# Kernel tuning notes

Measured on AMD Instinct MI355X. Metric: run time of the kernel, lower is better.

The kernel has to match this reference:

```python
import jax, jax.numpy as jnp
import numpy as np

B = 128
C_IN = 1
HID = 256
LAT = 256
NC = 4096
NA = 16
G = 4
DH = 256        # DynamicsModel default hidden_dim
CE = DH // 2    # code/action embed dim
IMG = 64
COMMIT = 0.25
DN = ('NCHW', 'OIHW', 'NCHW')


def conv_s2(x, w, b):
    y = jax.lax.conv_general_dilated(x, w, (2, 2), ((1, 1), (1, 1)), dimension_numbers=DN)
    return y + b[None, :, None, None]


def deconv_s2(x, w, b):
    # torch ConvTranspose2d(k=4, s=2, p=1): flip kernel, swap I/O channels,
    wt = jnp.flip(w, (2, 3)).transpose(1, 0, 2, 3)
    y = jax.lax.conv_general_dilated(x, wt, (1, 1), ((2, 2), (2, 2)),
                                     lhs_dilation=(2, 2), dimension_numbers=DN)
    return y + b[None, :, None, None]


def setup_inputs():
    key = jax.random.key(0)
    ks = iter(jax.random.split(key, 64))

    def W(shape, fan_in):
        return jax.random.normal(next(ks), shape, jnp.float32) * np.float32(1.0 / np.sqrt(fan_in))

    inp = {}
    inp['x'] = jax.random.uniform(next(ks), (B, C_IN, IMG, IMG), jnp.float32)
    inp['x_next'] = jax.random.uniform(next(ks), (B, C_IN, IMG, IMG), jnp.float32)
    inp['action'] = jax.random.randint(next(ks), (B,), 0, NA)
    # encoder Conv2d weights: [out, in, 4, 4]
    inp['enc_w1'] = W((HID, C_IN, 4, 4), C_IN * 16); inp['enc_b1'] = jnp.zeros((HID,), jnp.float32)
    inp['enc_w2'] = W((HID, HID, 4, 4), HID * 16);   inp['enc_b2'] = jnp.zeros((HID,), jnp.float32)
    inp['enc_w3'] = W((HID, HID, 4, 4), HID * 16);   inp['enc_b3'] = jnp.zeros((HID,), jnp.float32)
    inp['enc_w4'] = W((LAT, HID, 4, 4), HID * 16);   inp['enc_b4'] = jnp.zeros((LAT,), jnp.float32)
    # decoder ConvTranspose2d weights: [in, out, 4, 4]
    inp['dec_w1'] = W((LAT, HID, 4, 4), LAT * 4);    inp['dec_b1'] = jnp.zeros((HID,), jnp.float32)
    inp['dec_w2'] = W((HID, HID, 4, 4), HID * 4);    inp['dec_b2'] = jnp.zeros((HID,), jnp.float32)
    inp['dec_w3'] = W((HID, HID, 4, 4), HID * 4);    inp['dec_b3'] = jnp.zeros((HID,), jnp.float32)
    inp['dec_w4'] = W((HID, C_IN, 4, 4), HID * 4);   inp['dec_b4'] = jnp.zeros((C_IN,), jnp.float32)
    inp['codebook'] = jax.random.normal(next(ks), (NC, LAT), jnp.float32)
    inp['code_embed'] = W((NC, CE), CE)
    inp['action_embed'] = W((NA, CE), CE)
    d_in = G * G * CE + CE
    inp['dyn_w1'] = W((d_in, DH), d_in);      inp['dyn_b1'] = jnp.zeros((DH,), jnp.float32)
    inp['dyn_w2'] = W((DH, DH), DH);          inp['dyn_b2'] = jnp.zeros((DH,), jnp.float32)
    inp['dyn_w3'] = W((DH, G * G * NC), DH);  inp['dyn_b3'] = jnp.zeros((G * G * NC,), jnp.float32)
    return inp


def reference(x, x_next, action,
              enc_w1, enc_b1, enc_w2, enc_b2, enc_w3, enc_b3, enc_w4, enc_b4,
              dec_w1, dec_b1, dec_w2, dec_b2, dec_w3, dec_b3, dec_w4, dec_b4,
              codebook, code_embed, action_embed,
              dyn_w1, dyn_b1, dyn_w2, dyn_b2, dyn_w3, dyn_b3):
    relu = jax.nn.relu
    sg = jax.lax.stop_gradient

    cb_sq = jnp.sum(codebook * codebook, axis=1)  # [NC]

    def encode(xi):
        h = relu(conv_s2(xi, enc_w1, enc_b1))
        h = relu(conv_s2(h, enc_w2, enc_b2))
        h = relu(conv_s2(h, enc_w3, enc_b3))
        z = conv_s2(h, enc_w4, enc_b4)                   # [B, LAT, G, G]
        zf = z.transpose(0, 2, 3, 1).reshape(-1, LAT)    # [B*G*G, LAT]
        # squared euclidean distances (argmin identical to cdist argmin)
        d2 = jnp.sum(zf * zf, axis=1, keepdims=True) - 2.0 * (zf @ codebook.T) + cb_sq
        codes = jnp.argmin(d2, axis=-1)                  # [B*G*G]
        zq = codebook[codes]                             # [B*G*G, LAT]
        return zf, zq, codes

    zf, zq, codes_flat = encode(x)
    commitment_loss = jnp.mean((zf - sg(zq)) ** 2)
    codebook_loss = jnp.mean((sg(zf) - zq) ** 2)
    vq_loss = codebook_loss + COMMIT * commitment_loss
    zq_st = zf + sg(zq - zf)                             # straight-through

    zq_grid = zq_st.reshape(-1, G, G, LAT).transpose(0, 3, 1, 2)  # [B, LAT, G, G]
    codes = codes_flat.reshape(-1, G, G)

    # decoder
    h = relu(deconv_s2(zq_grid, dec_w1, dec_b1))
    h = relu(deconv_s2(h, dec_w2, dec_b2))
    h = relu(deconv_s2(h, dec_w3, dec_b3))
    recon = jax.nn.sigmoid(deconv_s2(h, dec_w4, dec_b4))  # [B, 1, 64, 64]

    # dynamics
    ce = code_embed[codes].reshape(codes.shape[0], -1)    # [B, G*G*CE]
    ae = action_embed[action]                             # [B, CE]
    h2 = jnp.concatenate([ce, ae], axis=-1)
    h2 = relu(h2 @ dyn_w1 + dyn_b1)
    h2 = relu(h2 @ dyn_w2 + dyn_b2)
    next_logits = (h2 @ dyn_w3 + dyn_b3).reshape(-1, G, G, NC)

    # next-code target (no grad in original)
    _, _, nc_flat = encode(sg(x_next))
    next_codes_target = nc_flat.reshape(-1, G, G)

    return (recon, codes, commitment_loss, codebook_loss, vq_loss,
            next_logits, next_codes_target)
```

## Files before the change

kernel.cpp:

```cpp
#include <hip/hip_runtime.h>
#include <hip/hip_bf16.h>

typedef _Float16 f16;
typedef f16   f16x8 __attribute__((ext_vector_type(8)));
typedef short s16x8 __attribute__((ext_vector_type(8)));
typedef float f32x4 __attribute__((ext_vector_type(4)));
typedef unsigned short u16;

__device__ __forceinline__ f32x4 mfma_f16(f16x8 a, f16x8 b, f32x4 c){
  return __builtin_amdgcn_mfma_f32_16x16x32_f16(a,b,c,0,0,0);
}
__device__ __forceinline__ f32x4 mfma_bf16(s16x8 a, s16x8 b, f32x4 c){
  return __builtin_amdgcn_mfma_f32_16x16x32_bf16(a,b,c,0,0,0);
}
__device__ __forceinline__ u16 f2bf(float v){
  unsigned u = __float_as_uint(v);
  unsigned r = u + 0x7fffu + ((u>>16)&1u);
  return (u16)(r>>16);
}
__device__ __forceinline__ float bf2f(u16 v){ return __uint_as_float(((unsigned)v)<<16); }

#define N_B 128

#define OUT_RECON 0
#define OUT_CODES 524288
#define OUT_LC    526336
#define OUT_NL    526339
#define OUT_NCT   8914947

#define B_E1H  0ull
#define B_E1L  67108864ull
#define B_ZF   67108864ull
#define B_ZQ4  69206016ull
#define B_ZSQ  70254592ull
#define B_ACC  70287360ull
#define B_CODES 70320128ull
#define B_H1   70385664ull
#define B_H2   70516736ull
#define B_H2B  70647808ull
#define B_E3H  71303168ull
#define B_E3L  75497472ull
#define B_D1   71303168ull
#define B_D2   75497472ull
#define B_EMB  92274688ull
#define B_ZFH  100663296ull
#define B_ZFL  101711872ull
#define B_E2H  134217728ull
#define B_E2L  150994944ull
#define B_DOTS 134217728ull
#define B_WE2H 167772160ull
#define B_WE2L 169869312ull
#define B_WE3H 171966464ull
#define B_WE3L 174063616ull
#define B_WE4H 176160768ull
#define B_WE4L 178257920ull
#define B_WD1  180355072ull
#define B_WD2  182452224ull
#define B_WD3  184549376ull
#define B_CBSQ 186646528ull
#define B_ZERO 186712064ull
#define B_CBH  186712576ull
#define B_CBL  188809728ull

__global__ __launch_bounds__(256) void k_pack_enc(const float* __restrict__ w,
                                                  f16* __restrict__ Wh, f16* __restrict__ Wl){
  int o = blockIdx.x*256 + threadIdx.x;
  int j=o&7, l=(o>>3)&63, n=(o>>9)&15, icc=(o>>13)&7, tap=o>>16;
  int ic = icc*32 + (l>>4)*8 + j, oc = n*16 + (l&15);
  float v = w[((size_t)oc*256+ic)*16 + tap];
  f16 h = (f16)v;
  Wh[o]=h; Wl[o]=(f16)(v-(float)h);
}
__global__ __launch_bounds__(256) void k_pack_dec(const float* __restrict__ w, u16* __restrict__ Wp){
  int o = blockIdx.x*256 + threadIdx.x;
  int j=o&7, l=(o>>3)&63, n=(o>>9)&15, icc=(o>>13)&7, tap=o>>16;
  int ic = icc*32 + (l>>4)*8 + j, oc = n*16 + (l&15);
  Wp[o] = f2bf(w[((size_t)ic*256+oc)*16 + tap]);
}
__global__ __launch_bounds__(256) void k_pack_cb(const float* __restrict__ cb,
                                                 f16* __restrict__ H, f16* __restrict__ L){
  int s = blockIdx.x*256 + threadIdx.x;
  int n = s>>8, k = s&255;
  float v = cb[s];
  int nt = n>>4, lr2 = n&15, icc = k>>5, rr = k&31, lq2 = rr>>3, j = rr&7;
  size_t o = ((size_t)(nt*8+icc)*64 + lq2*16 + lr2)*8 + j;
  f16 h = (f16)v; H[o]=h; L[o]=(f16)(v-(float)h);
}
__global__ __launch_bounds__(256) void k_cbsq(const float* __restrict__ cb, float* __restrict__ cbsq,
                                              float* __restrict__ zg){
  int c = blockIdx.x*256 + threadIdx.x;
  if(blockIdx.x==0 && threadIdx.x<128) zg[threadIdx.x]=0.f;
  const float4* r4 = (const float4*)(cb + (size_t)c*256);
  float s = 0.f;
  for(int k=0;k<64;k++){ float4 v=r4[k]; s += v.x*v.x+v.y*v.y+v.z*v.z+v.w*v.w; }
  cbsq[c] = s;
}

__global__ __launch_bounds__(256) void k_conv1(const float* __restrict__ x, const float* __restrict__ w1,
                                               const float* __restrict__ b1,
                                               f16* __restrict__ Oh, f16* __restrict__ Ol){
  int b = blockIdx.x >> 5, oy = blockIdx.x & 31;
  int oc = threadIdx.x;
  __shared__ float xs[4][68];
  for(int i=threadIdx.x;i<264;i+=256){
    int rr=i/66, cc=i-rr*66;
    int iy=2*oy-1+rr, ix=cc-1;
    float v=0.f;
    if((unsigned)iy<64u && (unsigned)ix<64u) v = x[((size_t)b*64+iy)*64+ix];
    xs[rr][cc]=v;
  }
  __syncthreads();
  float wv[16];
  #pragma unroll
  for(int k=0;k<16;k++) wv[k]=w1[oc*16+k];
  float bv=b1[oc];
  for(int ox=0;ox<32;ox++){
    float acc=bv;
    int c0=2*ox;
    #pragma unroll
    for(int kh=0;kh<4;kh++)
      #pragma unroll
      for(int kw=0;kw<4;kw++) acc += wv[kh*4+kw]*xs[kh][c0+kw];
    float v = fmaxf(acc,0.f);
    f16 h=(f16)v;
    size_t o = (((size_t)b*32+oy)*32+ox)*256+oc;
    Oh[o]=h; Ol[o]=(f16)(v-(float)h);
  }
}

template<int MT, int HIN>
__global__ __launch_bounds__(256,2) void k_conv_v2(
    const f16* __restrict__ Ah, const f16* __restrict__ Al,
    const f16* __restrict__ Wh, const f16* __restrict__ Wl,
    const float* __restrict__ bias, f16* __restrict__ Oh, f16* __restrict__ Ol){
  constexpr int HOUT = HIN/2, HH = HOUT*HOUT;
  constexpr int ROWS = MT*16, RS = 260;
  constexpr int REPS = MT*2;
  __shared__ f16 As[ROWS*RS];
  const int tid = threadIdx.x, lane = tid&63, w = tid>>6;
  const int lr = lane&15, lq = lane>>4;
  const int m_base = blockIdx.x*ROWS;
  int s_oy[REPS], s_ox[REPS], s_ls[REPS];
  size_t s_gb[REPS];
  #pragma unroll
  for(int rep=0;rep<REPS;rep++){
    int idx = rep*256 + tid;
    int ml = idx>>5, ch = idx&31;
    int m = m_base + ml;
    int b = m/HH, rem = m - b*HH;
    s_oy[rep] = rem/HOUT; s_ox[rep] = rem - s_oy[rep]*HOUT;
    s_gb[rep] = (size_t)b*HIN*HIN*256 + ch*8;
    s_ls[rep] = ml*RS + ch*8;
  }
  f32x4 acc[MT][4];
  #pragma unroll
  for(int t=0;t<MT;t++)
    #pragma unroll
    for(int u=0;u<4;u++) acc[t][u] = (f32x4){0.f,0.f,0.f,0.f};

  for(int tap=0;tap<16;tap++){
    const int th=tap>>2, tw=tap&3;
    __syncthreads();
    #pragma unroll
    for(int rep=0;rep<REPS;rep++){
      int iy = 2*s_oy[rep]-1+th, ix = 2*s_ox[rep]-1+tw;
      f16x8 v = {0,0,0,0,0,0,0,0};
      if((unsigned)iy<(unsigned)HIN && (unsigned)ix<(unsigned)HIN)
        v = *(const f16x8*)(Ah + s_gb[rep] + (size_t)(iy*HIN+ix)*256);
      *(f16x8*)&As[s_ls[rep]] = v;
    }
    __syncthreads();
    #pragma unroll
    for(int icc=0;icc<8;icc++){
      f16x8 a[MT];
      #pragma unroll
      for(int t=0;t<MT;t++) a[t] = *(const f16x8*)&As[(t*16+lr)*RS + lq*8 + icc*32];
      size_t wb = ((size_t)(tap*8+icc)*16 + w*4)*512 + lane*8;
      #pragma unroll
      for(int u=0;u<4;u++){
        f16x8 b_h = *(const f16x8*)(Wh + wb + u*512);
        f16x8 b_l = *(const f16x8*)(Wl + wb + u*512);
        #pragma unroll
        for(int t=0;t<MT;t++){
          acc[t][u] = mfma_f16(a[t], b_h, acc[t][u]);
          acc[t][u] = mfma_f16(a[t], b_l, acc[t][u]);
        }
      }
    }
    __syncthreads();
    #pragma unroll
    for(int rep=0;rep<REPS;rep++){
      int iy = 2*s_oy[rep]-1+th, ix = 2*s_ox[rep]-1+tw;
      f16x8 v = {0,0,0,0,0,0,0,0};
      if((unsigned)iy<(unsigned)HIN && (unsigned)ix<(unsigned)HIN)
        v = *(const f16x8*)(Al + s_gb[rep] + (size_t)(iy*HIN+ix)*256);
      *(f16x8*)&As[s_ls[rep]] = v;
    }
    __syncthreads();
    #pragma unroll
    for(int icc=0;icc<8;icc++){
      f16x8 a[MT];
      #pragma unroll
      for(int t=0;t<MT;t++) a[t] = *(const f16x8*)&As[(t*16+lr)*RS + lq*8 + icc*32];
      size_t wb = ((size_t)(tap*8+icc)*16 + w*4)*512 + lane*8;
      #pragma unroll
      for(int u=0;u<4;u++){
        f16x8 b_h = *(const f16x8*)(Wh + wb + u*512);
        #pragma unroll
        for(int t=0;t<MT;t++) acc[t][u] = mfma_f16(a[t], b_h, acc[t][u]);
      }
    }
  }
  #pragma unroll
  for(int t=0;t<MT;t++){
    #pragma unroll
    for(int u=0;u<4;u++){
      int n = (w*4+u)*16 + lr;
      float bv = bias[n];
      #pragma unroll
      for(int r=0;r<4;r++){
        int m = m_base + t*16 + lq*4 + r;
        float v = fmaxf(acc[t][u][r] + bv, 0.f);
        size_t o = (size_t)m*256 + n;
        f16 h=(f16)v; Oh[o]=h; Ol[o]=(f16)(v-(float)h);
      }
    }
  }
}

template<int MT>
__global__ __launch_bounds__(256) void k_conv4(
    const f16* __restrict__ Ah, const f16* __restrict__ Al,
    const f16* __restrict__ Wh, const f16* __restrict__ Wl,
    const float* __restrict__ bias, float* __restrict__ Of,
    f16* __restrict__ Zh, f16* __restrict__ Zl,
    const f16* __restrict__ Zp, int Hin){
  const int Hout = Hin>>1, HH = Hout*Hout;
  const int lane = threadIdx.x & 63, w = threadIdx.x >> 6;
  const int lr = lane & 15, lq = lane >> 4;
  const int m_base = blockIdx.x * (16*MT);
  int iyb[MT], ixb[MT], bb[MT];
  #pragma unroll
  for(int t=0;t<MT;t++){
    int m = m_base + t*16 + lr;
    int b = m/HH, rem = m - b*HH;
    int oy = rem/Hout, ox = rem - oy*Hout;
    bb[t]=b; iyb[t]=2*oy-1; ixb[t]=2*ox-1;
  }
  f32x4 acc[MT][4];
  #pragma unroll
  for(int t=0;t<MT;t++)
    #pragma unroll
    for(int u=0;u<4;u++) acc[t][u]=(f32x4){0.f,0.f,0.f,0.f};

  for(int tap=0;tap<16;tap++){
    int th=tap>>2, tw=tap&3;
    const f16* pH[MT]; const f16* pL[MT];
    #pragma unroll
    for(int t=0;t<MT;t++){
      int iy=iyb[t]+th, ix=ixb[t]+tw;
      bool val = ((unsigned)iy<(unsigned)Hin) && ((unsigned)ix<(unsigned)Hin);
      size_t o = (((size_t)bb[t]*Hin+iy)*Hin+ix)*256 + lq*8;
      pH[t] = val ? Ah+o : Zp;
      pL[t] = val ? Al+o : Zp;
    }
    #pragma unroll
    for(int icc=0;icc<8;icc++){
      f16x8 a_h[MT], a_l[MT];
      #pragma unroll
      for(int t=0;t<MT;t++){
        a_h[t] = *(const f16x8*)(pH[t] + icc*32);
        a_l[t] = *(const f16x8*)(pL[t] + icc*32);
      }
      size_t wb = ((size_t)(tap*8+icc)*16 + w*4)*512 + lane*8;
      #pragma unroll
      for(int u=0;u<4;u++){
        f16x8 b_h = *(const f16x8*)(Wh + wb + u*512);
        f16x8 b_l = *(const f16x8*)(Wl + wb + u*512);
        #pragma unroll
        for(int t=0;t<MT;t++){
          acc[t][u] = mfma_f16(a_h[t], b_h, acc[t][u]);
          acc[t][u] = mfma_f16(a_h[t], b_l, acc[t][u]);
          acc[t][u] = mfma_f16(a_l[t], b_h, acc[t][u]);
        }
      }
    }
  }
  #pragma unroll
  for(int t=0;t<MT;t++){
    #pragma unroll
    for(int u=0;u<4;u++){
      int n = (w*4+u)*16 + lr;
      float bv = bias[n];
      #pragma unroll
      for(int r=0;r<4;r++){
        int m = m_base + t*16 + lq*4 + r;
        float v = acc[t][u][r] + bv;
        size_t o = (size_t)m*256 + n;
        Of[o]=v;
        f16 h=(f16)v; Zh[o]=h; Zl[o]=(f16)(v-(float)h);
      }
    }
  }
}

template<int MT>
__global__ __launch_bounds__(256) void k_deconv_mfma(
    const u16* __restrict__ In, const u16* __restrict__ Wp,
    const float* __restrict__ bias, u16* __restrict__ Out,
    const u16* __restrict__ Zp, int H){
  const int Ho = H*2, HH = H*H;
  const int kh = blockIdx.y>>1, kw = blockIdx.y&1;
  const int lane = threadIdx.x & 63, w = threadIdx.x >> 6;
  const int lr = lane & 15, lq = lane >> 4;
  const int m_base = blockIdx.x * (16*MT);
  int jb[MT], ib[MT], bb[MT];
  #pragma unroll
  for(int t=0;t<MT;t++){
    int m = m_base + t*16 + lr;
    int b = m/HH, rem = m - b*HH;
    jb[t]=rem/H; ib[t]=rem-jb[t]*H; bb[t]=b;
  }
  f32x4 acc[MT][4];
  #pragma unroll
  for(int t=0;t<MT;t++)
    #pragma unroll
    for(int u=0;u<4;u++) acc[t][u]=(f32x4){0.f,0.f,0.f,0.f};

  #pragma unroll
  for(int dy=0;dy<2;dy++){
    #pragma unroll
    for(int dx=0;dx<2;dx++){
      int t16 = (kh+2*dy)*4 + (kw+2*dx);
      const u16* pA[MT];
      #pragma unroll
      for(int t=0;t<MT;t++){
        int r = jb[t]+(1-kh)-dy, c = ib[t]+(1-kw)-dx;
        bool val = ((unsigned)r<(unsigned)H) && ((unsigned)c<(unsigned)H);
        size_t o = (((size_t)bb[t]*H+r)*H+c)*256 + lq*8;
        pA[t] = val ? In+o : Zp;
      }
      #pragma unroll
      for(int icc=0;icc<8;icc++){
        s16x8 a[MT];
        #pragma unroll
        for(int t=0;t<MT;t++) a[t] = *(const s16x8*)(pA[t] + icc*32);
        size_t wb = ((size_t)(t16*8+icc)*16 + w*4)*512 + lane*8;
        #pragma unroll
        for(int u=0;u<4;u++){
          s16x8 bfr = *(const s16x8*)(Wp + wb + u*512);
          #pragma unroll
          for(int t=0;t<MT;t++) acc[t][u] = mfma_bf16(a[t], bfr, acc[t][u]);
        }
      }
    }
  }
  #pragma unroll
  for(int t=0;t<MT;t++){
    #pragma unroll
    for(int u=0;u<4;u++){
      int n = (w*4+u)*16 + lr;
      float bv = bias[n];
      #pragma unroll
      for(int r=0;r<4;r++){
        int m = m_base + t*16 + lq*4 + r;
        int b = m/HH, rem = m - b*HH;
        int j = rem/H, i = rem - j*H;
        int oy = 2*j + (1-kh), ox = 2*i + (1-kw);
        float v = fmaxf(acc[t][u][r] + bv, 0.f);
        Out[(((size_t)b*Ho+oy)*Ho+ox)*256 + n] = f2bf(v);
      }
    }
  }
}

__global__ __launch_bounds__(256) void k_dec4(const u16* __restrict__ In, const float* __restrict__ w4,
                                              const float* __restrict__ bias, float* __restrict__ out){
  __shared__ float wt[16][256];
  int t = threadIdx.x;
  for(int i=t;i<4096;i+=256) wt[i&15][i>>4] = w4[i];
  __syncthreads();
  int ox = t & 63, oy = (blockIdx.x<<2) + (t>>6), b = blockIdx.y;
  int iyh=(oy+1)>>1, kh=(oy+1)&1;
  int ixh=(ox+1)>>1, kw=(ox+1)&1;
  float acc = bias[0];
  #pragma unroll
  for(int dy=0;dy<2;dy++){
    int r = iyh-dy;
    if((unsigned)r>=32u) continue;
    #pragma unroll
    for(int dx=0;dx<2;dx++){
      int c = ixh-dx;
      if((unsigned)c>=32u) continue;
      const u16* p = In + (((size_t)b*32+r)*32+c)*256;
      int widx = (kh+2*dy)*4 + kw+2*dx;
      float s=0.f;
      for(int ic=0;ic<256;ic+=8){
        s16x8 vv = *(const s16x8*)(p+ic);
        const float* wr = &wt[widx][ic];
        #pragma unroll
        for(int q=0;q<8;q++) s += bf2f((u16)vv[q])*wr[q];
      }
      acc += s;
    }
  }
  out[(size_t)b*4096 + oy*64 + ox] = 1.f/(1.f+__expf(-acc));
}

__global__ __launch_bounds__(256) void k_zsq(const float* __restrict__ zf, float* __restrict__ zsq){
  int r=blockIdx.x, c=threadIdx.x;
  float v = zf[(size_t)r*256+c];
  __shared__ float red[256];
  red[c]=v*v; __syncthreads();
  for(int s=128;s>0;s>>=1){ if(c<s) red[c]+=red[c+s]; __syncthreads(); }
  if(c==0) zsq[r]=red[0];
}

__global__ __launch_bounds__(256,2) void k_dots(
    const f16* __restrict__ ZH, const f16* __restrict__ ZL,
    const f16* __restrict__ CH, const f16* __restrict__ CL, float* __restrict__ D){
  const int lane = threadIdx.x & 63, w = threadIdx.x >> 6;
  const int lr = lane & 15, lq = lane >> 4;
  const int m_base = blockIdx.y*64, nb = blockIdx.x;
  f32x4 acc[4][4];
  #pragma unroll
  for(int t=0;t<4;t++)
    #pragma unroll
    for(int u=0;u<4;u++) acc[t][u]=(f32x4){0.f,0.f,0.f,0.f};
  #pragma unroll
  for(int icc=0;icc<8;icc++){
    f16x8 ah[4], al[4];
    #pragma unroll
    for(int t=0;t<4;t++){
      size_t o = (size_t)(m_base + t*16 + lr)*256 + lq*8 + icc*32;
      ah[t] = *(const f16x8*)(ZH+o);
      al[t] = *(const f16x8*)(ZL+o);
    }
    #pragma unroll
    for(int u=0;u<4;u++){
      int nt = nb*16 + w*4 + u;
      size_t wb = ((size_t)(nt*8+icc)*64 + lane)*8;
      f16x8 b_h = *(const f16x8*)(CH+wb);
      f16x8 b_l = *(const f16x8*)(CL+wb);
      #pragma unroll
      for(int t=0;t<4;t++){
        acc[t][u] = mfma_f16(ah[t], b_h, acc[t][u]);
        acc[t][u] = mfma_f16(ah[t], b_l, acc[t][u]);
        acc[t][u] = mfma_f16(al[t], b_h, acc[t][u]);
      }
    }
  }
  #pragma unroll
  for(int t=0;t<4;t++)
    #pragma unroll
    for(int u=0;u<4;u++){
      int n = nb*256 + (w*4+u)*16 + lr;
      #pragma unroll
      for(int r=0;r<4;r++){
        int m = m_base + t*16 + lq*4 + r;
        D[(size_t)m*4096 + n] = acc[t][u][r];
      }
    }
}

__global__ __launch_bounds__(256) void k_argmin(const float* __restrict__ dots, const float* __restrict__ zsq,
                                                const float* __restrict__ cbsq, int* __restrict__ codes,
                                                float* __restrict__ out_codes){
  int r = blockIdx.x, t = threadIdx.x;
  float zs = zsq[r];
  float bv = 1e30f; int bi = 0x7fffffff;
  for(int c=t;c<4096;c+=256){
    float d = zs + cbsq[c] - 2.f*dots[(size_t)r*4096+c];
    if(d < bv || (d==bv && c<bi)){ bv=d; bi=c; }
  }
  __shared__ float sv[256]; __shared__ int si[256];
  sv[t]=bv; si[t]=bi; __syncthreads();
  for(int s=128;s>0;s>>=1){
    if(t<s){
      float v2=sv[t+s]; int i2=si[t+s];
      if(v2<sv[t] || (v2==sv[t] && i2<si[t])){ sv[t]=v2; si[t]=i2; }
    }
    __syncthreads();
  }
  if(t==0){ codes[r]=si[0]; out_codes[r]=(float)si[0]; }
}

__global__ void k_zero(float* a){ a[0]=0.f; }

__global__ __launch_bounds__(256) void k_zqloss(const float* __restrict__ zf, const float* __restrict__ cb,
                                                const int* __restrict__ codes, u16* __restrict__ zq4,
                                                float* __restrict__ accum){
  int r = blockIdx.x, c = threadIdx.x;
  int code = codes[r];
  float q = cb[(size_t)code*256 + c];
  float d = zf[(size_t)r*256+c] - q;
  zq4[(size_t)r*256 + c] = f2bf(q);
  __shared__ float red[256];
  red[c]=d*d; __syncthreads();
  for(int s=128;s>0;s>>=1){ if(c<s) red[c]+=red[c+s]; __syncthreads(); }
  if(c==0) atomicAdd(accum, red[0]);
}

__global__ void k_final(const float* __restrict__ accum, float* __restrict__ out){
  if(threadIdx.x==0){
    float L = accum[0]*(1.f/524288.f);
    out[0]=L; out[1]=L; out[2]=1.25f*L;
  }
}

__global__ __launch_bounds__(256) void k_embed(const int* __restrict__ codes, const int* __restrict__ action,
                                               const float* __restrict__ ce, const float* __restrict__ ae,
                                               float* __restrict__ emb){
  int b = blockIdx.x;
  for(int j=threadIdx.x;j<2176;j+=256){
    float v;
    if(j<2048){ int g=j>>7; v = ce[(size_t)codes[b*16+g]*128 + (j&127)]; }
    else      { v = ae[(size_t)action[b]*128 + (j-2048)]; }
    emb[(size_t)b*2176+j]=v;
  }
}

__global__ __launch_bounds__(256) void k_mlp(const float* __restrict__ in, const float* __restrict__ w,
                                             const float* __restrict__ bias, float* __restrict__ out,
                                             u16* __restrict__ outb, int K){
  int b = blockIdx.x, n = threadIdx.x;
  extern __shared__ float row[];
  for(int k=n;k<K;k+=256) row[k]=in[(size_t)b*K+k];
  __syncthreads();
  float acc = bias[n];
  for(int k=0;k<K;k++) acc += row[k]*w[(size_t)k*256+n];
  float v = fmaxf(acc,0.f);
  out[(size_t)b*256+n] = v;
  if(outb) outb[(size_t)b*256+n] = f2bf(v);
}

__global__ __launch_bounds__(256,2) void k_head(const u16* __restrict__ A,
                                                const float* __restrict__ w3,
                                                const float* __restrict__ b3,
                                                float* __restrict__ O){
  __shared__ u16 BS[8*64*8];
  const int tid = threadIdx.x, lane = tid&63, w = tid>>6;
  const int lr = lane&15, lq = lane>>4;
  const int nb = blockIdx.x;
  f32x4 acc[8][2];
  #pragma unroll
  for(int mt=0;mt<8;mt++)
    #pragma unroll
    for(int u=0;u<2;u++) acc[mt][u]=(f32x4){0.f,0.f,0.f,0.f};
  for(int icc=0;icc<8;icc++){
    __syncthreads();
    #pragma unroll
    for(int q=0;q<4;q++){
      int s = tid*16 + q*4;
      int kl = s>>7, nl = s&127;
      float4 v = *(const float4*)(w3 + (size_t)(icc*32+kl)*65536 + (size_t)nb*128 + nl);
      float vv[4] = {v.x,v.y,v.z,v.w};
      int j = kl&7, lqk = kl>>3;
      #pragma unroll
      for(int e=0;e<4;e++){
        int n2 = nl+e, ntl = n2>>4, lr2 = n2&15;
        BS[(ntl*64 + lqk*16 + lr2)*8 + j] = f2bf(vv[e]);
      }
    }
    __syncthreads();
    s16x8 a[8];
    #pragma unroll
    for(int mt=0;mt<8;mt++)
      a[mt] = *(const s16x8*)(A + (size_t)(mt*16+lr)*256 + icc*32 + lq*8);
    #pragma unroll
    for(int u=0;u<2;u++){
      int ntl = w*2+u;
      s16x8 bfr = *(const s16x8*)&BS[((size_t)ntl*64 + lane)*8];
      #pragma unroll
      for(int mt=0;mt<8;mt++) acc[mt][u] = mfma_bf16(a[mt], bfr, acc[mt][u]);
    }
  }
  #pragma unroll
  for(int mt=0;mt<8;mt++)
    #pragma unroll
    for(int u=0;u<2;u++){
      int n = nb*128 + (w*2+u)*16 + lr;
      float bv = b3[n];
      #pragma unroll
      for(int r=0;r<4;r++){
        int m = mt*16 + lq*4 + r;
        O[(size_t)m*65536 + n] = acc[mt][u][r] + bv;
      }
    }
}

extern "C" void kernel_launch(void* const* d_in, const int* in_sizes, int n_in,
                              void* d_out, int out_size, void* d_ws, size_t ws_size,
                              hipStream_t stream){
  (void)in_sizes; (void)n_in; (void)out_size; (void)ws_size;
  const float* x    = (const float*)d_in[0];
  const float* xn   = (const float*)d_in[1];
  const int*   act  = (const int*)  d_in[2];
  const float* ew1=(const float*)d_in[3];  const float* eb1=(const float*)d_in[4];
  const float* ew2=(const float*)d_in[5];  const float* eb2=(const float*)d_in[6];
  const float* ew3=(const float*)d_in[7];  const float* eb3=(const float*)d_in[8];
  const float* ew4=(const float*)d_in[9];  const float* eb4=(const float*)d_in[10];
  const float* dw1=(const float*)d_in[11]; const float* db1=(const float*)d_in[12];
  const float* dw2=(const float*)d_in[13]; const float* db2=(const float*)d_in[14];
  const float* dw3=(const float*)d_in[15]; const float* db3=(const float*)d_in[16];
  const float* dw4=(const float*)d_in[17]; const float* db4=(const float*)d_in[18];
  const float* cbk =(const float*)d_in[19];
  const float* cemb=(const float*)d_in[20];
  const float* aemb=(const float*)d_in[21];
  const float* yw1=(const float*)d_in[22]; const float* yb1=(const float*)d_in[23];
  const float* yw2=(const float*)d_in[24]; const float* yb2=(const float*)d_in[25];
  const float* yw3=(const float*)d_in[26]; const float* yb3=(const float*)d_in[27];
  float* out = (float*)d_out;

  char* wsb = (char*)d_ws;
  f16* E1H=(f16*)(wsb+B_E1H); f16* E1L=(f16*)(wsb+B_E1L);
  f16* E2H=(f16*)(wsb+B_E2H); f16* E2L=(f16*)(wsb+B_E2L);
  f16* E3H=(f16*)(wsb+B_E3H); f16* E3L=(f16*)(wsb+B_E3L);
  float* ZF=(float*)(wsb+B_ZF);
  f16* ZFH=(f16*)(wsb+B_ZFH); f16* ZFL=(f16*)(wsb+B_ZFL);
  u16* ZQ4=(u16*)(wsb+B_ZQ4);
  f16* WE2H=(f16*)(wsb+B_WE2H); f16* WE2L=(f16*)(wsb+B_WE2L);
  f16* WE3H=(f16*)(wsb+B_WE3H); f16* WE3L=(f16*)(wsb+B_WE3L);
  f16* WE4H=(f16*)(wsb+B_WE4H); f16* WE4L=(f16*)(wsb+B_WE4L);
  u16* WD1=(u16*)(wsb+B_WD1); u16* WD2=(u16*)(wsb+B_WD2); u16* WD3=(u16*)(wsb+B_WD3);
  f16* CBH=(f16*)(wsb+B_CBH); f16* CBL=(f16*)(wsb+B_CBL);
  float* ZSQ=(float*)(wsb+B_ZSQ); float* CBSQ=(float*)(wsb+B_CBSQ);
  float* EMB=(float*)(wsb+B_EMB); float* H1=(float*)(wsb+B_H1); float* H2=(float*)(wsb+B_H2);
  u16* H2B=(u16*)(wsb+B_H2B);
  float* ACC=(float*)(wsb+B_ACC); int* CODES=(int*)(wsb+B_CODES);
  float* ZG=(float*)(wsb+B_ZERO);
  const f16* Zf16=(const f16*)ZG; const u16* Zbf=(const u16*)ZG;
  float* DOTS=(float*)(wsb+B_DOTS);
  u16* D1=(u16*)(wsb+B_D1);
  u16* D2=(u16*)(wsb+B_D2);
  u16* D3=(u16*)(wsb+B_E1H);

  k_pack_enc<<<4096,256,0,stream>>>(ew2, WE2H, WE2L);
  k_pack_enc<<<4096,256,0,stream>>>(ew3, WE3H, WE3L);
  k_pack_enc<<<4096,256,0,stream>>>(ew4, WE4H, WE4L);
  k_pack_dec<<<4096,256,0,stream>>>(dw1, WD1);
  k_pack_dec<<<4096,256,0,stream>>>(dw2, WD2);
  k_pack_dec<<<4096,256,0,stream>>>(dw3, WD3);
  k_pack_cb <<<4096,256,0,stream>>>(cbk, CBH, CBL);
  k_cbsq<<<16,256,0,stream>>>(cbk, CBSQ, ZG);

  auto encode = [&](const float* img, float* code_out){
    k_conv1<<<4096,256,0,stream>>>(img, ew1, eb1, E1H, E1L);
    k_conv_v2<4,32><<<512,256,0,stream>>>(E1H,E1L, WE2H,WE2L, eb2, E2H,E2L);
    k_conv_v2<2,16><<<256,256,0,stream>>>(E2H,E2L, WE3H,WE3L, eb3, E3H,E3L);
    k_conv4<1><<<128,256,0,stream>>>(E3H,E3L, WE4H,WE4L, eb4, ZF, ZFH, ZFL, Zf16, 8);
    k_zsq<<<2048,256,0,stream>>>(ZF, ZSQ);
    k_dots<<<dim3(16,32),256,0,stream>>>(ZFH, ZFL, CBH, CBL, DOTS);
    k_argmin<<<2048,256,0,stream>>>(DOTS, ZSQ, CBSQ, CODES, code_out);
  };

  encode(x, out+OUT_CODES);
  k_zero<<<1,1,0,stream>>>(ACC);
  k_zqloss<<<2048,256,0,stream>>>(ZF, cbk, CODES, ZQ4, ACC);
  k_final<<<1,64,0,stream>>>(ACC, out+OUT_LC);

  k_deconv_mfma<1><<<dim3(128,4),256,0,stream>>>(ZQ4, WD1, db1, D1, Zbf, 4);
  k_deconv_mfma<4><<<dim3(128,4),256,0,stream>>>(D1,  WD2, db2, D2, Zbf, 8);
  k_deconv_mfma<4><<<dim3(512,4),256,0,stream>>>(D2,  WD3, db3, D3, Zbf, 16);
  k_dec4<<<dim3(16,N_B),256,0,stream>>>(D3, dw4, db4, out+OUT_RECON);

  k_embed<<<N_B,256,0,stream>>>(CODES, act, cemb, aemb, EMB);
  k_mlp<<<N_B,256,2176*4,stream>>>(EMB, yw1, yb1, H1, nullptr, 2176);
  k_mlp<<<N_B,256, 256*4,stream>>>(H1,  yw2, yb2, H2, H2B, 256);
  k_head<<<512,256,0,stream>>>(H2B, yw3, yb3, out+OUT_NL);

  encode(xn, out+OUT_NCT);
}
```

Baseline: 2.027 ms.

## Stage input halo patches per channel chunk to reuse across all 16 conv taps

The stride-2 encoder conv kernel now loops over 32-channel chunks outermost and loads a halo patch of input rows (hi and lo f16 parts) into shared memory once per chunk. All 16 kernel taps then read from that patch, where previously a separate im2col gather ran for every tap, once for the hi part and once for the lo part. The goal is to cut redundant global loads and the number of barriers. In exchange the kernel uses more shared memory, and the LDS padding stride changes bank behaviour. The third conv layer also switches to MT=1 with twice as many blocks.

Result: no change. 1.992 ms (-1.7%).

```diff
diff --git a/kernel.cpp b/kernel.cpp
--- a/kernel.cpp
+++ b/kernel.cpp
@@ -129,85 +129,82 @@
 }
 
 template<int MT, int HIN>
-__global__ __launch_bounds__(256,2) void k_conv_v2(
+__global__ __launch_bounds__(256,2) void k_conv_v3(
     const f16* __restrict__ Ah, const f16* __restrict__ Al,
     const f16* __restrict__ Wh, const f16* __restrict__ Wl,
     const float* __restrict__ bias, f16* __restrict__ Oh, f16* __restrict__ Ol){
   constexpr int HOUT = HIN/2, HH = HOUT*HOUT;
-  constexpr int ROWS = MT*16, RS = 260;
-  constexpr int REPS = MT*2;
-  __shared__ f16 As[ROWS*RS];
+  constexpr int ROWS = MT*16;
+  constexpr int OYS  = ROWS/HOUT;
+  static_assert(OYS*HOUT == ROWS, "block must cover whole oy rows");
+  constexpr int IYT = 2*OYS + 2;
+  constexpr int IXT = HIN + 2;
+  constexpr int XS  = 40;
+  constexpr int RS  = IXT*XS;
+  constexpr int BUF = IYT*RS;
+  constexpr int ITEMS = IYT*IXT*8;
+  __shared__ f16 As[2*BUF];
   const int tid = threadIdx.x, lane = tid&63, w = tid>>6;
   const int lr = lane&15, lq = lane>>4;
   const int m_base = blockIdx.x*ROWS;
-  int s_oy[REPS], s_ox[REPS], s_ls[REPS];
-  size_t s_gb[REPS];
-  #pragma unroll
-  for(int rep=0;rep<REPS;rep++){
-    int idx = rep*256 + tid;
-    int ml = idx>>5, ch = idx&31;
-    int m = m_base + ml;
-    int b = m/HH, rem = m - b*HH;
-    s_oy[rep] = rem/HOUT; s_ox[rep] = rem - s_oy[rep]*HOUT;
-    s_gb[rep] = (size_t)b*HIN*HIN*256 + ch*8;
-    s_ls[rep] = ml*RS + ch*8;
-  }
+  const int b = m_base/HH;
+  const int oy0 = (m_base - b*HH)/HOUT;
+  const int iy0 = 2*oy0 - 1;
+  const size_t gimg = (size_t)b*HIN*HIN*256;
+
+  int rb[MT];
+  #pragma unroll
+  for(int t=0;t<MT;t++){
+    int r = t*16 + lr;
+    int oyl = r/HOUT, oxl = r - oyl*HOUT;
+    rb[t] = (2*oyl)*RS + (2*oxl)*XS + lq*8;
+  }
+
   f32x4 acc[MT][4];
   #pragma unroll
   for(int t=0;t<MT;t++)
     #pragma unroll
     for(int u=0;u<4;u++) acc[t][u] = (f32x4){0.f,0.f,0.f,0.f};
 
-  for(int tap=0;tap<16;tap++){
-    const int th=tap>>2, tw=tap&3;
+  for(int icc=0;icc<8;icc++){
     __syncthreads();
-    #pragma unroll
-    for(int rep=0;rep<REPS;rep++){
-      int iy = 2*s_oy[rep]-1+th, ix = 2*s_ox[rep]-1+tw;
+    for(int s=tid;s<ITEMS;s+=256){
+      int c = s&7, posi = s>>3;
+      int hl = c>>2, ck = c&3;
+      int iyl = posi/IXT, ixl = posi - iyl*IXT;
+      int iy = iy0 + iyl, ix = ixl - 1;
       f16x8 v = {0,0,0,0,0,0,0,0};
-      if((unsigned)iy<(unsigned)HIN && (unsigned)ix<(unsigned)HIN)
-        v = *(const f16x8*)(Ah + s_gb[rep] + (size_t)(iy*HIN+ix)*256);
-      *(f16x8*)&As[s_ls[rep]] = v;
+      if((unsigned)iy<(unsigned)HIN && (unsigned)ix<(unsigned)HIN){
+        const f16* src = (hl ? Al : Ah) + gimg + (size_t)(iy*HIN+ix)*256 + icc*32 + ck*8;
+        v = *(const f16x8*)src;
+      }
+      *(f16x8*)&As[hl*BUF + iyl*RS + ixl*XS + ck*8] = v;
     }
     __syncthreads();
     #pragma unroll
-    for(int icc=0;icc<8;icc++){
-      f16x8 a[MT];
-      #pragma unroll
-      for(int t=0;t<MT;t++) a[t] = *(const f16x8*)&As[(t*16+lr)*RS + lq*8 + icc*32];
-      size_t wb = ((size_t)(tap*8+icc)*16 + w*4)*512 + lane*8;
-      #pragma unroll
-      for(int u=0;u<4;u++){
-        f16x8 b_h = *(const f16x8*)(Wh + wb + u*512);
-        f16x8 b_l = *(const f16x8*)(Wl + wb + u*512);
+    for(int th=0;th<4;th++){
+      #pragma unroll
+      for(int tw=0;tw<4;tw++){
+        const int tap = th*4 + tw;
+        f16x8 a_h[MT], a_l[MT];
         #pragma unroll
         for(int t=0;t<MT;t++){
-          acc[t][u] = mfma_f16(a[t], b_h, acc[t][u]);
-          acc[t][u] = mfma_f16(a[t], b_l, acc[t][u]);
+          int off = rb[t] + th*RS + tw*XS;
+          a_h[t] = *(const f16x8*)&As[off];
+          a_l[t] = *(const f16x8*)&As[BUF + off];
         }
-      }
-    }
-    __syncthreads();
-    #pragma unroll
-    for(int rep=0;rep<REPS;rep++){
-      int iy = 2*s_oy[rep]-1+th, ix = 2*s_ox[rep]-1+tw;
-      f16x8 v = {0,0,0,0,0,0,0,0};
-      if((unsigned)iy<(unsigned)HIN && (unsigned)ix<(unsigned)HIN)
-        v = *(const f16x8*)(Al + s_gb[rep] + (size_t)(iy*HIN+ix)*256);
-      *(f16x8*)&As[s_ls[rep]] = v;
-    }
-    __syncthreads();
-    #pragma unroll
-    for(int icc=0;icc<8;icc++){
-      f16x8 a[MT];
-      #pragma unroll
-      for(int t=0;t<MT;t++) a[t] = *(const f16x8*)&As[(t*16+lr)*RS + lq*8 + icc*32];
-      size_t wb = ((size_t)(tap*8+icc)*16 + w*4)*512 + lane*8;
-      #pragma unroll
-      for(int u=0;u<4;u++){
-        f16x8 b_h = *(const f16x8*)(Wh + wb + u*512);
+        size_t wb = ((size_t)(tap*8+icc)*16 + w*4)*512 + lane*8;
         #pragma unroll
-        for(int t=0;t<MT;t++) acc[t][u] = mfma_f16(a[t], b_h, acc[t][u]);
+        for(int u=0;u<4;u++){
+          f16x8 b_h = *(const f16x8*)(Wh + wb + u*512);
+          f16x8 b_l = *(const f16x8*)(Wl + wb + u*512);
+          #pragma unroll
+          for(int t=0;t<MT;t++){
+            acc[t][u] = mfma_f16(a_h[t], b_h, acc[t][u]);
+            acc[t][u] = mfma_f16(a_h[t], b_l, acc[t][u]);
+            acc[t][u] = mfma_f16(a_l[t], b_h, acc[t][u]);
+          }
+        }
       }
     }
   }
@@ -646,8 +643,8 @@
 
   auto encode = [&](const float* img, float* code_out){
     k_conv1<<<4096,256,0,stream>>>(img, ew1, eb1, E1H, E1L);
-    k_conv_v2<4,32><<<512,256,0,stream>>>(E1H,E1L, WE2H,WE2L, eb2, E2H,E2L);
-    k_conv_v2<2,16><<<256,256,0,stream>>>(E2H,E2L, WE3H,WE3L, eb3, E3H,E3L);
+    k_conv_v3<4,32><<<512,256,0,stream>>>(E1H,E1L, WE2H,WE2L, eb2, E2H,E2L);
+    k_conv_v3<1,16><<<512,256,0,stream>>>(E2H,E2L, WE3H,WE3L, eb3, E3H,E3L);
     k_conv4<1><<<128,256,0,stream>>>(E3H,E3L, WE4H,WE4L, eb4, ZF, ZFH, ZFL, Zf16, 8);
     k_zsq<<<2048,256,0,stream>>>(ZF, ZSQ);
     k_dots<<<dim3(16,32),256,0,stream>>>(ZFH, ZFL, CBH, CBL, DOTS);
```
